# Kernel optimization log

Measured on AMD Instinct MI355X. Metric: run time of the kernel, lower is better.

The kernel has to match this reference:

```python
import jax, jax.numpy as jnp
import numpy as np

B, S, D = 2, 1024, 4096
NQ, NKV, HD = 32, 8, 128
G = NQ // NKV
FFN = 10928  # ffn_size(4096, 4.0): int(4*4096)*2//3 = 10922 -> round up to mult of 8
ATTN_MULT = 0.08838834764831845
MAX_ATTN = 30.0
EPS = 1e-5
BASE = 10000.0


def setup_inputs() -> dict:
    key = jax.random.key(0)
    ks = jax.random.split(key, 13)
    def w(k, shape):
        return jax.random.normal(k, shape, jnp.float32) / np.float32(np.sqrt(shape[0]))
    return {
        "x": jax.random.normal(ks[0], (B, S, D), jnp.float32),
        "mask": jnp.tril(jnp.ones((1, 1, S, S), dtype=bool)),  # causal
        "scale_pre_attn": jax.random.uniform(ks[1], (D,), jnp.float32, 0.5, 1.5),
        "scale_post_attn": jax.random.uniform(ks[2], (D,), jnp.float32, 0.5, 1.5),
        "scale_pre_mlp": jax.random.uniform(ks[3], (D,), jnp.float32, 0.5, 1.5),
        "scale_post_mlp": jax.random.uniform(ks[4], (D,), jnp.float32, 0.5, 1.5),
        "wq": w(ks[5], (D, NQ * HD)),
        "wk": w(ks[6], (D, NKV * HD)),
        "wv": w(ks[7], (D, NKV * HD)),
        "wo": w(ks[8], (NQ * HD, D)),
        "w_gate": w(ks[9], (D, FFN)),
        "w_val": w(ks[10], (D, FFN)),
        "w_out": w(ks[11], (FFN, D)),
    }


def rms_norm(x, scale):
    ms = jnp.mean(jnp.square(x), axis=-1, keepdims=True)
    return x * jax.lax.rsqrt(ms + EPS) * scale


def rotate_half(x):
    x1, x2 = jnp.split(x, 2, axis=-1)
    return jnp.concatenate((-x2, x1), axis=-1)


def apply_rope(x):
    # x: [b, s, h, d]; offset=0 (no KV-cache step)
    s, d = x.shape[1], x.shape[3]
    inv_freq = 1.0 / (BASE ** (jnp.arange(0, d, 2, dtype=jnp.float32) / d))
    t = jnp.arange(s, dtype=jnp.float32)
    phase = t[:, None] * inv_freq[None, :]            # [s, d/2]
    phase = jnp.tile(phase, (1, 2))[None, :, None, :]  # [1, s, 1, d]
    return (x * jnp.cos(phase) + rotate_half(x) * jnp.sin(phase)).astype(x.dtype)


def reference(x, mask, scale_pre_attn, scale_post_attn, scale_pre_mlp, scale_post_mlp,
              wq, wk, wv, wo, w_gate, w_val, w_out):
    h = x
    # ---- attention sublayer (pre-norm) ----
    hn = rms_norm(h, scale_pre_attn)
    q = (hn @ wq).reshape(B, S, NQ, HD)
    k = (hn @ wk).reshape(B, S, NKV, HD)
    v = (hn @ wv).reshape(B, S, NKV, HD)
    q = apply_rope(q)
    k = apply_rope(k)
    qg = q.reshape(B, S, NKV, G, HD)  # GQA: group q heads per kv head
    logits = jnp.einsum("btkgd,bskd->bkgts", qg, k).astype(jnp.float32) * ATTN_MULT
    logits = MAX_ATTN * jnp.tanh(logits / MAX_ATTN)   # grok soft cap
    logits = jnp.where(mask[:, :, None], logits, -1e30)
    probs = jax.nn.softmax(logits, axis=-1).astype(x.dtype)
    attn = jnp.einsum("bkgts,bskd->btkgd", probs, v).reshape(B, S, NQ * HD)
    h_attn = attn @ wo
    h = h + rms_norm(h_attn, scale_post_attn)
    # ---- gated MLP sublayer (pre-norm) ----
    hn2 = rms_norm(h, scale_pre_mlp)
    h_dense = (jax.nn.gelu(hn2 @ w_gate) * (hn2 @ w_val)) @ w_out
    h = h + rms_norm(h_dense, scale_post_mlp)
    return h
```

## Files before the change

### kernel.cpp

```cpp
#include <hip/hip_runtime.h>
#include <stdint.h>

typedef unsigned short ushort_t;
typedef unsigned short us8 __attribute__((ext_vector_type(8)));
typedef __bf16 bf16x8 __attribute__((ext_vector_type(8)));
typedef float f32x4 __attribute__((ext_vector_type(4)));

#define D_MODEL 4096
#define SEQ 1024
#define BROWS 2048
#define QKV_N 6144
#define HD 128
#define FFN_GRID 11008
#define ATTN_MULT 0.08838834764831845f

__device__ __forceinline__ unsigned short f2bf(float f){
  union { float f; unsigned u; } c; c.f = f;
  unsigned u = c.u + 0x7fffu + ((c.u >> 16) & 1u);
  return (unsigned short)(u >> 16);
}
__device__ __forceinline__ float bf2f(unsigned short h){
  union { unsigned u; float f; } c; c.u = ((unsigned)h) << 16;
  return c.f;
}
__device__ __forceinline__ f32x4 zero4(){ f32x4 z; z[0]=0.f; z[1]=0.f; z[2]=0.f; z[3]=0.f; return z; }
__device__ __forceinline__ bf16x8 ldb8(const void* p){ return *(const bf16x8*)p; }
__device__ __forceinline__ f32x4 MFMA(bf16x8 a, bf16x8 b, f32x4 c){
  return __builtin_amdgcn_mfma_f32_16x16x32_bf16(a, b, c, 0, 0, 0);
}
__device__ __forceinline__ void g2lds16(void* lds, const void* g){
  __builtin_amdgcn_global_load_lds(
      (const __attribute__((address_space(1))) void*)(uintptr_t)(g),
      (__attribute__((address_space(3))) void*)(uint32_t)(uintptr_t)(lds),
      16, 0, 0);
}
#define BAR() __builtin_amdgcn_s_barrier()
#define VMCNT8() asm volatile("s_waitcnt vmcnt(8)" ::: "memory")
#define VMCNT7() asm volatile("s_waitcnt vmcnt(7)" ::: "memory")
#define VMCNT0() asm volatile("s_waitcnt vmcnt(0)" ::: "memory")
#define LGKM0() asm volatile("s_waitcnt lgkmcnt(0)" ::: "memory")

__global__ __launch_bounds__(256) void rmsnorm_in(const float* __restrict__ x,
                                                  const float* __restrict__ sc,
                                                  ushort_t* __restrict__ out){
  int row = blockIdx.x, tid = threadIdx.x;
  const float4* xr = (const float4*)(x + (size_t)row*D_MODEL);
  float4 v[4]; float ss = 0.f;
#pragma unroll
  for (int i=0;i<4;i++){
    v[i] = xr[tid + i*256];
    ss += v[i].x*v[i].x + v[i].y*v[i].y + v[i].z*v[i].z + v[i].w*v[i].w;
  }
#pragma unroll
  for (int m=32;m;m>>=1) ss += __shfl_xor(ss, m);
  __shared__ float red[4];
  if ((tid&63)==0) red[tid>>6] = ss;
  __syncthreads();
  float inv = rsqrtf((red[0]+red[1]+red[2]+red[3])*(1.f/4096.f) + 1e-5f);
  const float4* scv = (const float4*)sc;
#pragma unroll
  for (int i=0;i<4;i++){
    float4 s4 = scv[tid + i*256];
    ushort4 o;
    o.x = f2bf(v[i].x*inv*s4.x); o.y = f2bf(v[i].y*inv*s4.y);
    o.z = f2bf(v[i].z*inv*s4.z); o.w = f2bf(v[i].w*inv*s4.w);
    ((ushort4*)out)[(size_t)row*1024 + tid + i*256] = o;
  }
}

__global__ __launch_bounds__(256) void rmsnorm_resid(const float* __restrict__ base,
                                                     const float* __restrict__ delta,
                                                     const float* __restrict__ delta2,
                                                     const float* __restrict__ sc1,
                                                     float* __restrict__ hout,
                                                     const float* __restrict__ sc2,
                                                     ushort_t* __restrict__ hn2){
  int row = blockIdx.x, tid = threadIdx.x;
  const float4* dr = (const float4*)(delta + (size_t)row*D_MODEL);
  const float4* d2 = delta2 ? (const float4*)(delta2 + (size_t)row*D_MODEL) : nullptr;
  const float4* br = (const float4*)(base  + (size_t)row*D_MODEL);
  float4 d[4]; float ss = 0.f;
#pragma unroll
  for (int i=0;i<4;i++){
    float4 a = dr[tid + i*256];
    if (d2){
      float4 b = d2[tid + i*256];
      a.x += b.x; a.y += b.y; a.z += b.z; a.w += b.w;
    }
    d[i] = a;
    ss += d[i].x*d[i].x + d[i].y*d[i].y + d[i].z*d[i].z + d[i].w*d[i].w;
  }
#pragma unroll
  for (int m=32;m;m>>=1) ss += __shfl_xor(ss, m);
  __shared__ float red[4];
  if ((tid&63)==0) red[tid>>6] = ss;
  __syncthreads();
  float inv1 = rsqrtf((red[0]+red[1]+red[2]+red[3])*(1.f/4096.f) + 1e-5f);
  const float4* s1v = (const float4*)sc1;
  float4* ho = (float4*)(hout + (size_t)row*D_MODEL);
  float4 h4[4]; float ss2 = 0.f;
#pragma unroll
  for (int i=0;i<4;i++){
    float4 b4 = br[tid + i*256];
    float4 s4 = s1v[tid + i*256];
    float4 h;
    h.x = b4.x + d[i].x*inv1*s4.x;
    h.y = b4.y + d[i].y*inv1*s4.y;
    h.z = b4.z + d[i].z*inv1*s4.z;
    h.w = b4.w + d[i].w*inv1*s4.w;
    h4[i] = h;
    ho[tid + i*256] = h;
    ss2 += h.x*h.x + h.y*h.y + h.z*h.z + h.w*h.w;
  }
  if (sc2){
#pragma unroll
    for (int m=32;m;m>>=1) ss2 += __shfl_xor(ss2, m);
    __syncthreads();
    if ((tid&63)==0) red[tid>>6] = ss2;
    __syncthreads();
    float inv2 = rsqrtf((red[0]+red[1]+red[2]+red[3])*(1.f/4096.f) + 1e-5f);
    const float4* s2v = (const float4*)sc2;
#pragma unroll
    for (int i=0;i<4;i++){
      float4 s4 = s2v[tid + i*256];
      ushort4 o;
      o.x = f2bf(h4[i].x*inv2*s4.x); o.y = f2bf(h4[i].y*inv2*s4.y);
      o.z = f2bf(h4[i].z*inv2*s4.z); o.w = f2bf(h4[i].w*inv2*s4.w);
      ((ushort4*)hn2)[(size_t)row*1024 + tid + i*256] = o;
    }
  }
}

__global__ __launch_bounds__(256) void convT(const float* __restrict__ W,
                                             ushort_t* __restrict__ WT,
                                             int K, int N, int Kp, int Np){
  __shared__ float tile[64][69];
  int tx = threadIdx.x & 15, ty = threadIdx.x >> 4;
  int n0 = blockIdx.x*64, k0 = blockIdx.y*64;
#pragma unroll
  for (int i=0;i<4;i++){
    int k = k0 + ty + i*16, n = n0 + tx*4;
    float4 v;
    if (k < K && n + 3 < N){
      v = *(const float4*)&W[(size_t)k*N + n];
    } else {
      v.x = (k<K && n+0<N) ? W[(size_t)k*N + n+0] : 0.f;
      v.y = (k<K && n+1<N) ? W[(size_t)k*N + n+1] : 0.f;
      v.z = (k<K && n+2<N) ? W[(size_t)k*N + n+2] : 0.f;
      v.w = (k<K && n+3<N) ? W[(size_t)k*N + n+3] : 0.f;
    }
    tile[ty+i*16][tx*4+0] = v.x;
    tile[ty+i*16][tx*4+1] = v.y;
    tile[ty+i*16][tx*4+2] = v.z;
    tile[ty+i*16][tx*4+3] = v.w;
  }
  __syncthreads();
  int kc = (threadIdx.x & 7)*8, nr = threadIdx.x >> 3;
#pragma unroll
  for (int j=0;j<2;j++){
    int n = n0 + nr + j*32;
    if (n < Np){
      us8 o;
#pragma unroll
      for (int i=0;i<8;i++) o[i] = f2bf(tile[kc+i][nr + j*32]);
      *(us8*)&WT[(size_t)n*Kp + k0 + kc] = o;
    }
  }
}

template<int MODE, int KS, int CF>
__global__ __launch_bounds__(512, 2) void gemmW(const ushort_t* __restrict__ A, int lda,
                                                const ushort_t* __restrict__ WT, int ldw,
                                                void* __restrict__ Cv, void* __restrict__ Cv2,
                                                int ldc, int Nvalid, int K){
  constexpr int BN   = CF*32;
  constexpr int NCH  = 4 + CF/2;
  constexpr int SLOT = 32768 + (CF/2)*8192;
  __shared__ __align__(16) char smem[2*SLOT];
  const int nwg = gridDim.x;
  const int lid = blockIdx.x;
  int t = (lid & 7) * (nwg >> 3) + (lid >> 3);
  void* Cout = Cv;
  if (KS == 2){
    const int per = nwg >> 1;
    if (t >= per){ t -= per; A += (size_t)K; WT += (size_t)K; Cout = Cv2; }
  }
  const int m0 = (t & 7) << 8;
  const int n0 = (t >> 3) * BN;
  const int tid = threadIdx.x;
  const int w = tid >> 6, lane = tid & 63;
  const int wm = w >> 1, wn = w & 1;
  const int lo = lane & 15, hi = lane >> 4;
  const int srow = lane >> 3, scol = lane & 7;
  const int sw = scol ^ srow;
  const int rsw = lo & 7;
  const int NT = K >> 6;

  const ushort_t* pA = A  + (size_t)(m0 + w*8 + srow) * lda + sw*8;
  const ushort_t* pB = WT + (size_t)(n0 + w*8 + srow) * ldw + sw*8;

  auto stage = [&](int tt, int c){
    const ushort_t* g = (c < 4 ? pA + (size_t)(c*64)*lda : pB + (size_t)((c-4)*64)*ldw) + (size_t)tt*64;
    g2lds16(smem + (tt&1)*SLOT + (c < 4 ? c*8192 : 32768 + (c-4)*8192) + (w<<10), g);
  };

  f32x4 acc[4][CF];
#pragma unroll
  for (int i=0;i<4;i++)
#pragma unroll
    for (int j=0;j<CF;j++) acc[i][j] = zero4();

#pragma unroll
  for (int c=0;c<NCH;c++) stage(0, c);
#pragma unroll
  for (int c=0;c<NCH;c++) stage(1, c);

  for (int i=0;i<NT;i++){
    if (i == NT-1) { VMCNT0(); }
    else if (CF == 8) { VMCNT8(); } else { VMCNT7(); }
    BAR();
    const char* sA = smem + (i&1)*SLOT;
    const char* sB = sA + 32768;
    bf16x8 af[4][2], bfr[CF][2];
#pragma unroll
    for (int rf=0;rf<4;rf++)
#pragma unroll
      for (int kc=0;kc<2;kc++)
        af[rf][kc] = ldb8(sA + (wm*64 + rf*16 + lo)*128 + (((kc*4+hi)^rsw)<<4));
#pragma unroll
    for (int cf=0;cf<CF;cf++)
#pragma unroll
      for (int kc=0;kc<2;kc++)
        bfr[cf][kc] = ldb8(sB + (wn*(CF*16) + cf*16 + lo)*128 + (((kc*4+hi)^rsw)<<4));
    LGKM0();
    BAR();
    if (i+2 < NT){
#pragma unroll
      for (int c=0;c<NCH;c++) stage(i+2, c);
    }
#pragma unroll
    for (int rf=0;rf<4;rf++)
#pragma unroll
      for (int cf=0;cf<CF;cf++)
#pragma unroll
        for (int kc=0;kc<2;kc++)
          acc[rf][cf] = MFMA(af[rf][kc], bfr[cf][kc], acc[rf][cf]);
  }
#pragma unroll
  for (int rf=0;rf<4;rf++){
#pragma unroll
    for (int cf=0;cf<CF;cf++){
#pragma unroll
      for (int r=0;r<4;r++){
        int m = m0 + wm*64 + rf*16 + hi*4 + r;
        int n = n0 + wn*(CF*16) + cf*16 + lo;
        if (n < Nvalid){
          float v = acc[rf][cf][r];
          size_t idx = (size_t)m*ldc + n;
          if (MODE == 1) ((float*)Cout)[idx] = v;
          else           ((ushort_t*)Cout)[idx] = f2bf(v);
        }
      }
    }
  }
}

__global__ __launch_bounds__(512, 2) void gemm_gv(const ushort_t* __restrict__ A, int lda,
                                                  const ushort_t* __restrict__ B1,
                                                  const ushort_t* __restrict__ B2, int ldw,
                                                  ushort_t* __restrict__ Cv, int ldc,
                                                  int Nvalid, int K){
  __shared__ __align__(16) char smem[131072];
  const int nwg = gridDim.x;
  const int lid = blockIdx.x;
  const int t  = (lid & 7) * (nwg >> 3) + (lid >> 3);
  const int m0 = (t & 7) << 8;
  const int n0 = (t >> 3) << 7;
  const int tid = threadIdx.x;
  const int w = tid >> 6, lane = tid & 63;
  const int wm = w >> 1, wn = w & 1;
  const int lo = lane & 15, hi = lane >> 4;
  const int srow = lane >> 3, scol = lane & 7;
  const int sw = scol ^ srow;
  const int rsw = lo & 7;
  const int NT = K >> 6;

  const ushort_t* pA  = A  + (size_t)(m0 + w*8 + srow) * lda + sw*8;
  const ushort_t* pB1 = B1 + (size_t)(n0 + w*8 + srow) * ldw + sw*8;
  const ushort_t* pB2 = B2 + (size_t)(n0 + w*8 + srow) * ldw + sw*8;

  auto stage = [&](int tt, int c){
    const ushort_t* g;
    int lofs;
    if (c < 4){ g = pA  + (size_t)(c*64)*lda;     lofs = c*8192; }
    else if (c < 6){ g = pB1 + (size_t)((c-4)*64)*ldw; lofs = 32768 + (c-4)*8192; }
    else { g = pB2 + (size_t)((c-6)*64)*ldw; lofs = 49152 + (c-6)*8192; }
    g2lds16(smem + ((tt&1)<<16) + lofs + (w<<10), g + (size_t)tt*64);
  };

  f32x4 ag[4][4], av[4][4];
#pragma unroll
  for (int i=0;i<4;i++)
#pragma unroll
    for (int j=0;j<4;j++){ ag[i][j] = zero4(); av[i][j] = zero4(); }

#pragma unroll
  for (int c=0;c<8;c++) stage(0, c);
#pragma unroll
  for (int c=0;c<8;c++) stage(1, c);

  for (int i=0;i<NT;i++){
    if (i == NT-1) VMCNT0(); else VMCNT8();
    BAR();
    const char* sA  = smem + ((i&1)<<16);
    const char* sB1 = sA + 32768;
    const char* sB2 = sA + 49152;
    bf16x8 af[4][2], b1f[4][2], b2f[4][2];
#pragma unroll
    for (int rf=0;rf<4;rf++)
#pragma unroll
      for (int kc=0;kc<2;kc++)
        af[rf][kc] = ldb8(sA + (wm*64 + rf*16 + lo)*128 + (((kc*4+hi)^rsw)<<4));
#pragma unroll
    for (int cf=0;cf<4;cf++)
#pragma unroll
      for (int kc=0;kc<2;kc++){
        b1f[cf][kc] = ldb8(sB1 + (wn*64 + cf*16 + lo)*128 + (((kc*4+hi)^rsw)<<4));
        b2f[cf][kc] = ldb8(sB2 + (wn*64 + cf*16 + lo)*128 + (((kc*4+hi)^rsw)<<4));
      }
    LGKM0();
    BAR();
    if (i+2 < NT){
#pragma unroll
      for (int c=0;c<8;c++) stage(i+2, c);
    }
#pragma unroll
    for (int rf=0;rf<4;rf++)
#pragma unroll
      for (int cf=0;cf<4;cf++)
#pragma unroll
        for (int kc=0;kc<2;kc++){
          ag[rf][cf] = MFMA(af[rf][kc], b1f[cf][kc], ag[rf][cf]);
          av[rf][cf] = MFMA(af[rf][kc], b2f[cf][kc], av[rf][cf]);
        }
  }
#pragma unroll
  for (int rf=0;rf<4;rf++){
#pragma unroll
    for (int cf=0;cf<4;cf++){
#pragma unroll
      for (int r=0;r<4;r++){
        int m = m0 + wm*64 + rf*16 + hi*4 + r;
        int n = n0 + wn*64 + cf*16 + lo;
        if (n < Nvalid){
          float g = ag[rf][cf][r];
          float v = av[rf][cf][r];
          float ga = 0.5f*g*(1.f + tanhf(0.7978845608028654f*(g + 0.044715f*g*g*g)));
          Cv[(size_t)m*ldc + n] = f2bf(ga * v);
        }
      }
    }
  }
}

__global__ void rope_tab_kernel(float* __restrict__ tab){
  int s = blockIdx.x, i = threadIdx.x;
  float invf = __expf(-(float)i * (9.210340371976184f/64.f));
  float ph = (float)s * invf;
  float sn, cs;
  sincosf(ph, &sn, &cs);
  tab[s*128 + i] = cs;
  tab[s*128 + 64 + i] = sn;
}

__global__ __launch_bounds__(256) void rope_apply(ushort_t* __restrict__ qkv,
                                                  const float* __restrict__ tab){
  int idx = blockIdx.x*256 + threadIdx.x;
  int pr = idx & 63;
  int h  = (idx >> 6) % 40;
  int row = idx / 2560;
  int t = row & (SEQ-1);
  ushort_t* p = qkv + (size_t)row*QKV_N + h*HD + pr;
  float c = tab[t*128 + pr], s = tab[t*128 + 64 + pr];
  float x1 = bf2f(p[0]), x2 = bf2f(p[64]);
  p[0]  = f2bf(x1*c - x2*s);
  p[64] = f2bf(x2*c + x1*s);
}

__global__ __launch_bounds__(256) void transpose_v(const ushort_t* __restrict__ qkv,
                                                   ushort_t* __restrict__ VT){
  __shared__ ushort_t tile[32][33];
  int d0 = blockIdx.x*32, m0 = blockIdx.y*32;
  int tx = threadIdx.x & 31, ty = threadIdx.x >> 5;
#pragma unroll
  for (int i=0;i<4;i++)
    tile[ty + i*8][tx] = qkv[(size_t)(m0 + ty + i*8)*QKV_N + 5120 + d0 + tx];
  __syncthreads();
#pragma unroll
  for (int i=0;i<4;i++)
    VT[(size_t)(d0 + ty + i*8)*BROWS + m0 + tx] = tile[tx][ty + i*8];
}

__global__ __launch_bounds__(256) void attn_kernel(const ushort_t* __restrict__ qkv,
                                                   const ushort_t* __restrict__ VT,
                                                   ushort_t* __restrict__ outp){
  const int blk = blockIdx.x;
  const int bh = blk & 63;
  const int tgrp = 15 - (blk >> 6);
  const int b = bh >> 5, qh = bh & 31, kv = qh >> 2;
  const int w = threadIdx.x >> 6, lane = threadIdx.x & 63;
  const int lo = lane & 15, hi = lane >> 4;
  const int t0 = tgrp*64 + w*16;
  __shared__ ushort_t P[4][16][72];
  ushort_t (*Pw)[72] = P[w];

  const ushort_t* Qb = qkv + (size_t)(b*SEQ + t0 + lo)*QKV_N + qh*HD + hi*8;
  bf16x8 qf[4];
#pragma unroll
  for (int c=0;c<4;c++) qf[c] = ldb8(Qb + c*32);

  f32x4 of[8];
#pragma unroll
  for (int i=0;i<8;i++) of[i] = zero4();
  float ls[4] = {0.f,0.f,0.f,0.f};

  const ushort_t* Kb = qkv + (size_t)(b*SEQ + lo)*QKV_N + D_MODEL + kv*HD + hi*8;
  const ushort_t* Vb = VT + (size_t)(kv*HD + lo)*BROWS + b*SEQ + hi*8;

  const int nst = tgrp + 1;
  for (int st=0; st<nst; st++){
    const int s0 = st*64;
    f32x4 sacc[4];
#pragma unroll
    for (int nf=0;nf<4;nf++) sacc[nf] = zero4();
#pragma unroll
    for (int c=0;c<4;c++){
#pragma unroll
      for (int nf=0;nf<4;nf++){
        bf16x8 kf = ldb8(Kb + (size_t)(s0 + nf*16)*QKV_N + c*32);
        sacc[nf] = MFMA(qf[c], kf, sacc[nf]);
      }
    }
#pragma unroll
    for (int nf=0;nf<4;nf++){
#pragma unroll
      for (int r=0;r<4;r++){
        int tq = t0 + hi*4 + r;
        int s = s0 + nf*16 + lo;
        float xx = sacc[nf][r] * ATTN_MULT;
        float z = fminf(fmaxf(xx*(2.f/30.f), -80.f), 80.f);
        float e = __expf(z);
        float th = (e - 1.f)/(e + 1.f);
        float p = (s <= tq) ? __expf(30.f*th - 30.f) : 0.f;
        ls[r] += p;
        Pw[hi*4+r][nf*16+lo] = f2bf(p);
      }
    }
    __builtin_amdgcn_sched_barrier(0);
    __builtin_amdgcn_s_waitcnt(0xc07f);
    __builtin_amdgcn_sched_barrier(0);
#pragma unroll
    for (int c2=0;c2<2;c2++){
      bf16x8 pf = ldb8(&Pw[lo][c2*32 + hi*8]);
#pragma unroll
      for (int nf2=0;nf2<8;nf2++){
        bf16x8 vf = ldb8(Vb + (size_t)(nf2*16)*BROWS + s0 + c2*32);
        of[nf2] = MFMA(pf, vf, of[nf2]);
      }
    }
    __builtin_amdgcn_sched_barrier(0);
  }
#pragma unroll
  for (int m=1;m<16;m<<=1){
#pragma unroll
    for (int r=0;r<4;r++) ls[r] += __shfl_xor(ls[r], m);
  }
  float inv[4];
#pragma unroll
  for (int r=0;r<4;r++) inv[r] = 1.f/ls[r];
  ushort_t* Ob = outp + (size_t)(b*SEQ + t0 + hi*4)*D_MODEL + qh*HD + lo;
#pragma unroll
  for (int nf2=0;nf2<8;nf2++)
#pragma unroll
    for (int r=0;r<4;r++)
      Ob[(size_t)r*D_MODEL + nf2*16] = f2bf(of[nf2][r]*inv[r]);
}

extern "C" void kernel_launch(void* const* d_in, const int* in_sizes, int n_in,
                              void* d_out, int out_size, void* d_ws, size_t ws_size,
                              hipStream_t stream){
  const float* x        = (const float*)d_in[0];
  const float* sc_pre_a = (const float*)d_in[2];
  const float* sc_post_a= (const float*)d_in[3];
  const float* sc_pre_m = (const float*)d_in[4];
  const float* sc_post_m= (const float*)d_in[5];
  const float* wq  = (const float*)d_in[6];
  const float* wk  = (const float*)d_in[7];
  const float* wv  = (const float*)d_in[8];
  const float* wo  = (const float*)d_in[9];
  const float* wg  = (const float*)d_in[10];
  const float* wva = (const float*)d_in[11];
  const float* wou = (const float*)d_in[12];

  char* ws = (char*)d_ws;
  size_t off = 0;
  auto alloc = [&](size_t bytes)->void*{
    void* p = ws + off; off += (bytes + 255) & ~(size_t)255; return p;
  };
  ushort_t* WT   = (ushort_t*)alloc((size_t)FFN_GRID*D_MODEL*2);
  ushort_t* hn   = (ushort_t*)alloc((size_t)BROWS*D_MODEL*2);
  ushort_t* qkv  = (ushort_t*)alloc((size_t)BROWS*QKV_N*2);
  ushort_t* VT   = (ushort_t*)alloc((size_t)SEQ*BROWS*2);
  ushort_t* attn = (ushort_t*)alloc((size_t)BROWS*D_MODEL*2);
  float*    tmp32= (float*)alloc((size_t)BROWS*D_MODEL*4);
  ushort_t* hn2  = (ushort_t*)alloc((size_t)BROWS*D_MODEL*2);
  ushort_t* act  = (ushort_t*)alloc((size_t)BROWS*FFN_GRID*2);
  float*    rtab = (float*)alloc((size_t)SEQ*128*4);
  float* h = (float*)d_out;
  ushort_t* WT2  = (ushort_t*)hn;
  float* part_o  = (float*)act;
  float* part_u  = (float*)hn;

  rmsnorm_in<<<BROWS, 256, 0, stream>>>(x, sc_pre_a, hn);
  convT<<<dim3(64, 64), 256, 0, stream>>>(wq, WT,                     4096, 4096, 4096, 4096);
  convT<<<dim3(16, 64), 256, 0, stream>>>(wk, WT + (size_t)4096*4096, 4096, 1024, 4096, 1024);
  convT<<<dim3(16, 64), 256, 0, stream>>>(wv, WT + (size_t)5120*4096, 4096, 1024, 4096, 1024);
  gemmW<0,1,6><<<256, 512, 0, stream>>>(hn, 4096, WT, 4096, qkv, nullptr, QKV_N, QKV_N, 4096);
  rope_tab_kernel<<<SEQ, 64, 0, stream>>>(rtab);
  rope_apply<<<(BROWS*40*64)/256, 256, 0, stream>>>(qkv, rtab);
  transpose_v<<<dim3(32,64), 256, 0, stream>>>(qkv, VT);
  attn_kernel<<<1024, 256, 0, stream>>>(qkv, VT, attn);
  convT<<<dim3(64, 64), 256, 0, stream>>>(wo, WT, 4096, 4096, 4096, 4096);
  gemmW<1,2,8><<<256, 512, 0, stream>>>(attn, 4096, WT, 4096, tmp32, part_o, 4096, 4096, 2048);
  rmsnorm_resid<<<BROWS, 256, 0, stream>>>(x, tmp32, part_o, sc_post_a, h, sc_pre_m, hn2);
  convT<<<dim3(172, 64), 256, 0, stream>>>(wg,  WT,  4096, 10928, 4096, FFN_GRID);
  convT<<<dim3(172, 64), 256, 0, stream>>>(wva, WT2, 4096, 10928, 4096, FFN_GRID);
  gemm_gv<<<688, 512, 0, stream>>>(hn2, 4096, WT, WT2, 4096, act, FFN_GRID, FFN_GRID, 4096);
  convT<<<dim3(64, 172), 256, 0, stream>>>(wou, WT, 10928, 4096, FFN_GRID, 4096);
  gemmW<1,2,8><<<256, 512, 0, stream>>>(act, FFN_GRID, WT, FFN_GRID, tmp32, part_u, 4096, 4096, 5504);
  rmsnorm_resid<<<BROWS, 256, 0, stream>>>(h, tmp32, part_u, sc_post_m, h, nullptr, nullptr);
}
```

Measured before the change: 1.105 ms.

## Add small-tile split-K GEMM kernel for output projections to raise occupancy

Adds a new gemmS kernel with 256x128 tiles, K-step 32, 48KB LDS and launch bounds allowing 4 blocks per CU. It replaces gemmW for the attention output and MLP down projections, launching 512 blocks in a 2-way split-K. The aim is to fill more CUs and overlap loads across more resident workgroups than the large-tile kernel did. The cost is a shallower K step per barrier, which means more synchronisation, and a different traffic pattern. Half of the blocks also start with a short sleep to stagger their start.

```diff
diff --git a/kernel.cpp b/kernel.cpp
--- a/kernel.cpp
+++ b/kernel.cpp
@@ -37,6 +37,7 @@
 #define BAR() __builtin_amdgcn_s_barrier()
 #define VMCNT8() asm volatile("s_waitcnt vmcnt(8)" ::: "memory")
 #define VMCNT7() asm volatile("s_waitcnt vmcnt(7)" ::: "memory")
+#define VMCNT3() asm volatile("s_waitcnt vmcnt(3)" ::: "memory")
 #define VMCNT0() asm volatile("s_waitcnt vmcnt(0)" ::: "memory")
 #define LGKM0() asm volatile("s_waitcnt lgkmcnt(0)" ::: "memory")
 
@@ -254,6 +255,95 @@
       for (int r=0;r<4;r++){
         int m = m0 + wm*64 + rf*16 + hi*4 + r;
         int n = n0 + wn*(CF*16) + cf*16 + lo;
+        if (n < Nvalid){
+          float v = acc[rf][cf][r];
+          size_t idx = (size_t)m*ldc + n;
+          if (MODE == 1) ((float*)Cout)[idx] = v;
+          else           ((ushort_t*)Cout)[idx] = f2bf(v);
+        }
+      }
+    }
+  }
+}
+
+template<int MODE, int KS>
+__global__ __launch_bounds__(512, 4) void gemmS(const ushort_t* __restrict__ A, int lda,
+                                                const ushort_t* __restrict__ WT, int ldw,
+                                                void* __restrict__ Cv, void* __restrict__ Cv2,
+                                                int ldc, int Nvalid, int K){
+  __shared__ __align__(16) char smem[49152];
+  const int nwg = gridDim.x;
+  const int lid = blockIdx.x;
+  int t = (lid & 7) * (nwg >> 3) + (lid >> 3);
+  void* Cout = Cv;
+  if (KS == 2){
+    const int per = nwg >> 1;
+    if (t >= per){ t -= per; A += (size_t)K; WT += (size_t)K; Cout = Cv2; }
+  }
+  const int m0 = (t & 7) << 8;
+  const int n0 = (t >> 3) << 7;
+  const int tid = threadIdx.x;
+  const int w = tid >> 6, lane = tid & 63;
+  const int wm = w >> 1, wn = w & 1;
+  const int lo = lane & 15, hi = lane >> 4;
+  const int rsw2 = (lo >> 1) & 3;
+  const int strow = tid >> 2;
+  const int sseg  = (tid & 3) ^ ((tid >> 3) & 3);
+  const int NT = K >> 5;
+
+  auto stage = [&](int tt, int c){
+    const ushort_t* g;
+    int lofs;
+    if (c < 2){ g = A  + (size_t)(m0 + c*128 + strow)*lda; lofs = c*8192; }
+    else      { g = WT + (size_t)(n0 + strow)*ldw;         lofs = 16384; }
+    g2lds16(smem + (tt&1)*24576 + lofs + (w<<10),
+            g + (size_t)tt*32 + sseg*8);
+  };
+
+  f32x4 acc[4][4];
+#pragma unroll
+  for (int i=0;i<4;i++)
+#pragma unroll
+    for (int j=0;j<4;j++) acc[i][j] = zero4();
+
+#pragma unroll
+  for (int c=0;c<3;c++) stage(0, c);
+#pragma unroll
+  for (int c=0;c<3;c++) stage(1, c);
+
+  if (blockIdx.x & 256) __builtin_amdgcn_s_sleep(24);
+
+  for (int i=0;i<NT;i++){
+    if (i == NT-1) VMCNT0(); else VMCNT3();
+    BAR();
+    const char* sA = smem + (i&1)*24576;
+    const char* sB = sA + 16384;
+    bf16x8 af[4], bfr[4];
+#pragma unroll
+    for (int rf=0;rf<4;rf++)
+      af[rf] = ldb8(sA + (wm*64 + rf*16 + lo)*64 + ((hi^rsw2)<<4));
+#pragma unroll
+    for (int cf=0;cf<4;cf++)
+      bfr[cf] = ldb8(sB + (wn*64 + cf*16 + lo)*64 + ((hi^rsw2)<<4));
+    LGKM0();
+    BAR();
+    if (i+2 < NT){
+      stage(i+2, 0); stage(i+2, 1); stage(i+2, 2);
+    }
+#pragma unroll
+    for (int rf=0;rf<4;rf++)
+#pragma unroll
+      for (int cf=0;cf<4;cf++)
+        acc[rf][cf] = MFMA(af[rf], bfr[cf], acc[rf][cf]);
+  }
+#pragma unroll
+  for (int rf=0;rf<4;rf++){
+#pragma unroll
+    for (int cf=0;cf<4;cf++){
+#pragma unroll
+      for (int r=0;r<4;r++){
+        int m = m0 + wm*64 + rf*16 + hi*4 + r;
+        int n = n0 + wn*64 + cf*16 + lo;
         if (n < Nvalid){
           float v = acc[rf][cf][r];
           size_t idx = (size_t)m*ldc + n;
@@ -531,12 +621,12 @@
   transpose_v<<<dim3(32,64), 256, 0, stream>>>(qkv, VT);
   attn_kernel<<<1024, 256, 0, stream>>>(qkv, VT, attn);
   convT<<<dim3(64, 64), 256, 0, stream>>>(wo, WT, 4096, 4096, 4096, 4096);
-  gemmW<1,2,8><<<256, 512, 0, stream>>>(attn, 4096, WT, 4096, tmp32, part_o, 4096, 4096, 2048);
+  gemmS<1,2><<<512, 512, 0, stream>>>(attn, 4096, WT, 4096, tmp32, part_o, 4096, 4096, 2048);
   rmsnorm_resid<<<BROWS, 256, 0, stream>>>(x, tmp32, part_o, sc_post_a, h, sc_pre_m, hn2);
   convT<<<dim3(172, 64), 256, 0, stream>>>(wg,  WT,  4096, 10928, 4096, FFN_GRID);
   convT<<<dim3(172, 64), 256, 0, stream>>>(wva, WT2, 4096, 10928, 4096, FFN_GRID);
   gemm_gv<<<688, 512, 0, stream>>>(hn2, 4096, WT, WT2, 4096, act, FFN_GRID, FFN_GRID, 4096);
   convT<<<dim3(64, 172), 256, 0, stream>>>(wou, WT, 10928, 4096, FFN_GRID, 4096);
-  gemmW<1,2,8><<<256, 512, 0, stream>>>(act, FFN_GRID, WT, FFN_GRID, tmp32, part_u, 4096, 4096, 5504);
+  gemmS<1,2><<<512, 512, 0, stream>>>(act, FFN_GRID, WT, FFN_GRID, tmp32, part_u, 4096, 4096, 5504);
   rmsnorm_resid<<<BROWS, 256, 0, stream>>>(h, tmp32, part_u, sc_post_m, h, nullptr, nullptr);
 }
```

New measurement: 1.183 ms. 1.07x slower.
